# Optimization experiments

Measured on AMD Instinct MI355X. Metric: run time of the kernel, lower is better.

## Reference

```python
import jax, jax.numpy as jnp
import numpy as np

Q = 8192      # num query tokens
S = 32768     # num support points
E = 131072    # num edges (query<-support neighbor pairs)
D = 256       # token_dim
H = 8         # num_heads
HD = D // H   # head_dim = 32
GEO = 128     # geo mlp_hidden = geo_dim
FFN = 2 * D   # ffn hidden
STAT_IN = 12  # 4 stats * 3 coords
EPS_LN = 1e-5


def gelu(x):
    return jax.nn.gelu(x, approximate=False)  # torch nn.GELU default (erf)


def layernorm(x, g, b):
    m = jnp.mean(x, axis=-1, keepdims=True)
    v = jnp.mean((x - m) ** 2, axis=-1, keepdims=True)
    return (x - m) * jax.lax.rsqrt(v + EPS_LN) * g + b


def setup_inputs() -> dict:
    key = jax.random.key(0)
    ks = jax.random.split(key, 16)
    w = lambda k, shp: jax.random.normal(k, shp, jnp.float32) * 0.02
    return {
        "query_tokens": jax.random.normal(ks[0], (Q, D), jnp.float32),
        "query_pos": jax.random.normal(ks[1], (Q, 3), jnp.float32),
        "support_feats": jax.random.normal(ks[2], (S, D), jnp.float32),
        "support_pos": jax.random.normal(ks[3], (S, 3), jnp.float32),
        "Wq": w(ks[4], (D, D)), "Wk": w(ks[5], (D, D)), "Wv": w(ks[6], (D, D)),
        "Wg": w(ks[7], (GEO, D)),
        "Wo": w(ks[8], (D, D)), "bo": jnp.zeros((D,), jnp.float32),
        "log_tau": jnp.array(0.0, jnp.float32),
        "ln1_g": jnp.ones((D,), jnp.float32), "ln1_b": jnp.zeros((D,), jnp.float32),
        "ln2_g": jnp.ones((D,), jnp.float32), "ln2_b": jnp.zeros((D,), jnp.float32),
        "Wf1": w(ks[9], (D, FFN)), "bf1": jnp.zeros((FFN,), jnp.float32),
        "Wf2": w(ks[10], (FFN, D)), "bf2": jnp.zeros((D,), jnp.float32),
        "Gw1": w(ks[11], (STAT_IN, GEO)), "Gb1": jnp.zeros((GEO,), jnp.float32),
        "Gw2": w(ks[12], (GEO, GEO)), "Gb2": jnp.zeros((GEO,), jnp.float32),
        "q_idx": jnp.sort(jax.random.randint(ks[13], (E,), 0, Q)),
        "s_idx": jax.random.randint(ks[14], (E,), 0, S),
        "num_queries": Q,
    }


def geo_stats(rel, q_idx, num_q):
    # rel: [E,3] relative positions; segmented mean/std/min/max -> [num_q, 12]
    ones = jnp.ones((rel.shape[0], 1), rel.dtype)
    cnt = jnp.maximum(jax.ops.segment_sum(ones, q_idx, num_q), 1.0)  # [Q,1]
    mean = jax.ops.segment_sum(rel, q_idx, num_q) / cnt
    var = jax.ops.segment_sum((rel - mean[q_idx]) ** 2, q_idx, num_q) / cnt
    std = jnp.sqrt(var)
    # torch inits min/max with +/-inf then clamps to [-100,100]; jax segment
    # min/max init with dtype extremes -> same result after clip
    mn = jnp.clip(jax.ops.segment_min(rel, q_idx, num_q), -100.0, 100.0)
    mx = jnp.clip(jax.ops.segment_max(rel, q_idx, num_q), -100.0, 100.0)
    return jnp.concatenate([mean, std, mn, mx], axis=-1)


def reference(query_tokens, query_pos, support_feats, support_pos,
              Wq, Wk, Wv, Wg, Wo, bo, log_tau,
              ln1_g, ln1_b, ln2_g, ln2_b,
              Wf1, bf1, Wf2, bf2, Gw1, Gb1, Gw2, Gb2,
              q_idx, s_idx, num_queries):
    num_q = num_queries
    # ---- statistical geo embedding ----
    rel = support_pos[s_idx] - query_pos[q_idx]                 # [E,3]
    raw = geo_stats(rel, q_idx, num_q)                          # [Q,12]
    geo = gelu(gelu(raw @ Gw1 + Gb1) @ Gw2 + Gb2)               # [Q,GEO]

    # ---- AGNO cross attention (pre-norm) ----
    qt = layernorm(query_tokens, ln1_g, ln1_b)
    Qf = qt @ Wq                                                # [Q,D]
    Kf = support_feats @ Wk                                     # [S,D]
    Vf = support_feats @ Wv                                     # [S,D]
    Gf = geo @ Wg                                               # [Q,D]
    qh = Qf[q_idx].reshape(E, H, HD)
    kh = Kf[s_idx].reshape(E, H, HD)
    vh = Vf[s_idx].reshape(E, H, HD)
    gh = Gf[q_idx].reshape(E, H, HD)
    tau = jnp.exp(log_tau)
    scores = jnp.sum(qh * kh, axis=-1) / (jnp.sqrt(jnp.float32(HD)) * tau)  # [E,H]
    # torch scores_max starts at 0 -> max(0, segment max)
    smax = jnp.maximum(jax.ops.segment_max(scores, q_idx, num_q), 0.0)
    ex = jnp.exp(scores - smax[q_idx])
    ssum = jax.ops.segment_sum(ex, q_idx, num_q)
    alpha = ex / jnp.maximum(ssum[q_idx], 1e-8)                 # [E,H]
    weighted = alpha[..., None] * (vh + gh)                     # [E,H,HD]
    out = jax.ops.segment_sum(weighted, q_idx, num_q)           # [Q,H,HD]
    attn = out.reshape(num_q, D) @ Wo + bo

    # ---- residual + FFN ----
    x = query_tokens + attn
    x = x + gelu(layernorm(x, ln2_g, ln2_b) @ Wf1 + bf1) @ Wf2 + bf2
    return x
```

## Files before the change

### kernel.cpp

```cpp
#include <hip/hip_runtime.h>
#include <math.h>

#define QN 8192
#define SN 32768
#define EN 131072
#define DN 256
#define HN 8
#define HDN 32
#define GEON 128
#define FFNN 512

typedef __attribute__((ext_vector_type(8))) short bf16x8;
typedef __attribute__((ext_vector_type(8))) unsigned short u16x8;
typedef __attribute__((ext_vector_type(4))) float f32x4;

__device__ __forceinline__ unsigned short f2b(float f) {
  union { float f; unsigned u; } v; v.f = f;
  unsigned u = v.u;
  u += 0x7fffu + ((u >> 16) & 1u);
  return (unsigned short)(u >> 16);
}
__device__ __forceinline__ float b2f(unsigned short h) {
  union { unsigned u; float f; } v; v.u = ((unsigned)h) << 16; return v.f;
}
__device__ __forceinline__ float gelu_f(float x) {
  return 0.5f * x * (1.0f + erff(x * 0.70710678118654752440f));
}

template <int KT>
__device__ __forceinline__ u16x8* lds_gk(unsigned short* base, int row, int col) {
  int g = (col >> 3) ^ (row & 7);
  return reinterpret_cast<u16x8*>(base + row * KT + g * 8);
}
__device__ __forceinline__ unsigned short* lds_gs128(unsigned short* base, int row, int col) {
  int g = (col >> 3) ^ (row & 7);
  return base + row * 128 + g * 8 + (col & 7);
}

__global__ __launch_bounds__(256) void fused_prep(
    const float* Wq, const float* Wk, const float* Wv, const float* Wg,
    const float* Wo, const float* Wf1, const float* Wf2,
    unsigned short* WqT, unsigned short* WkvT, unsigned short* WgT,
    unsigned short* WoT, unsigned short* Wf1T, unsigned short* Wf2T,
    const int* q_idx, int* offs,
    const float* x_ln, const float* lng, const float* lnb, unsigned short* ln_out) {
  __shared__ float ts[64][65];
  int b = blockIdx.x;
  int t = threadIdx.x;
  if (b < 136) {
    const float* src; unsigned short* dst; int K, N, tile;
    if (b < 16)       { src = Wq;  dst = WqT;          K = 256; N = 256; tile = b; }
    else if (b < 32)  { src = Wk;  dst = WkvT;         K = 256; N = 256; tile = b - 16; }
    else if (b < 48)  { src = Wv;  dst = WkvT + 65536; K = 256; N = 256; tile = b - 32; }
    else if (b < 56)  { src = Wg;  dst = WgT;          K = 128; N = 256; tile = b - 48; }
    else if (b < 72)  { src = Wo;  dst = WoT;          K = 256; N = 256; tile = b - 56; }
    else if (b < 104) { src = Wf1; dst = Wf1T;         K = 256; N = 512; tile = b - 72; }
    else              { src = Wf2; dst = Wf2T;         K = 512; N = 256; tile = b - 104; }
    int ktiles = K >> 6;
    int k0 = (tile % ktiles) * 64, n0 = (tile / ktiles) * 64;
    int c4 = (t & 15) * 4;
    int r = t >> 4;
#pragma unroll
    for (int p = 0; p < 4; ++p) {
      int row = p * 16 + r;
      float4 v = *(const float4*)(src + (size_t)(k0 + row) * N + n0 + c4);
      ts[row][c4 + 0] = v.x; ts[row][c4 + 1] = v.y;
      ts[row][c4 + 2] = v.z; ts[row][c4 + 3] = v.w;
    }
    __syncthreads();
#pragma unroll
    for (int p = 0; p < 4; ++p) {
      int n = p * 16 + r;
      ushort4 o;
      o.x = f2b(ts[c4 + 0][n]); o.y = f2b(ts[c4 + 1][n]);
      o.z = f2b(ts[c4 + 2][n]); o.w = f2b(ts[c4 + 3][n]);
      *(ushort4*)(dst + (size_t)(n0 + n) * K + k0 + c4) = o;
    }
  } else if (b < 169) {
    int i = (b - 136) * 256 + t;
    if (i > QN) return;
    int lo = 0, hi = EN;
    while (lo < hi) {
      int mid = (lo + hi) >> 1;
      if (q_idx[mid] < i) lo = mid + 1; else hi = mid;
    }
    offs[i] = lo;
  } else {
    int row = (b - 169) * 4 + (t >> 6);
    int lane = t & 63;
    const float* xr = x_ln + (size_t)row * DN;
    float4 v = *(const float4*)(xr + lane * 4);
    float s = v.x + v.y + v.z + v.w;
    float ss = v.x * v.x + v.y * v.y + v.z * v.z + v.w * v.w;
#pragma unroll
    for (int msk = 1; msk <= 32; msk <<= 1) {
      s += __shfl_xor(s, msk);
      ss += __shfl_xor(ss, msk);
    }
    float mean = s * (1.f / 256.f);
    float var = ss * (1.f / 256.f) - mean * mean;
    float rs = 1.0f / sqrtf(var + 1e-5f);
    float4 gg = *(const float4*)(lng + lane * 4);
    float4 bb = *(const float4*)(lnb + lane * 4);
    unsigned short* o = ln_out + (size_t)row * DN + lane * 4;
    o[0] = f2b((v.x - mean) * rs * gg.x + bb.x);
    o[1] = f2b((v.y - mean) * rs * gg.y + bb.y);
    o[2] = f2b((v.z - mean) * rs * gg.z + bb.z);
    o[3] = f2b((v.w - mean) * rs * gg.w + bb.w);
  }
}

__global__ __launch_bounds__(256) void ln_kernel(
    const float* x, const float* g, const float* b, unsigned short* out) {
  int row = blockIdx.x * 4 + (threadIdx.x >> 6);
  int lane = threadIdx.x & 63;
  const float* xr = x + (size_t)row * DN;
  float4 v = *(const float4*)(xr + lane * 4);
  float s = v.x + v.y + v.z + v.w;
  float ss = v.x * v.x + v.y * v.y + v.z * v.z + v.w * v.w;
#pragma unroll
  for (int msk = 1; msk <= 32; msk <<= 1) {
    s += __shfl_xor(s, msk);
    ss += __shfl_xor(ss, msk);
  }
  float mean = s * (1.f / 256.f);
  float var = ss * (1.f / 256.f) - mean * mean;
  float rs = 1.0f / sqrtf(var + 1e-5f);
  float4 gg = *(const float4*)(g + lane * 4);
  float4 bb = *(const float4*)(b + lane * 4);
  unsigned short* o = out + (size_t)row * DN + lane * 4;
  o[0] = f2b((v.x - mean) * rs * gg.x + bb.x);
  o[1] = f2b((v.y - mean) * rs * gg.y + bb.y);
  o[2] = f2b((v.z - mean) * rs * gg.z + bb.z);
  o[3] = f2b((v.w - mean) * rs * gg.w + bb.w);
}


__device__ __forceinline__ void kv_body(
    char* smem, const float* A, const unsigned short* BT, unsigned short* KVb,
    int bm, int t) {
  unsigned short* As = (unsigned short*)smem;
  unsigned short* Bs = (unsigned short*)(smem + 32768);
  int w = t >> 6, lane = t & 63;
  int quad = lane >> 4, l16 = lane & 15;
  int wr = w >> 1, wc = w & 1;
  {
    int prow = t >> 6;
    int c4 = (t & 63) * 4;
#pragma unroll
    for (int p = 0; p < 16; ++p) {
      int lr = p * 4 + prow;
      float4 f = *(const float4*)(A + (size_t)(bm + lr) * 256 + c4);
      ushort4 u;
      u.x = f2b(f.x); u.y = f2b(f.y); u.z = f2b(f.z); u.w = f2b(f.w);
      int g = (c4 >> 3) ^ (lr & 7);
      *(ushort4*)(As + lr * 256 + g * 8 + (c4 & 7)) = u;
    }
  }
  int brow = t >> 3, bsub = t & 7;
  u16x8 pre[4];
  {
    const unsigned short* Bg = BT + (size_t)brow * 256 + bsub * 32;
#pragma unroll
    for (int i = 0; i < 4; ++i) pre[i] = *reinterpret_cast<const u16x8*>(Bg + i * 8);
  }
  for (int ct = 0; ct < 16; ++ct) {
#pragma unroll
    for (int i = 0; i < 4; ++i)
      *lds_gk<256>(Bs, brow, bsub * 32 + i * 8) = pre[i];
    __syncthreads();
    if (ct < 15) {
      const unsigned short* Bg = BT + (size_t)((ct + 1) * 32 + brow) * 256 + bsub * 32;
#pragma unroll
      for (int i = 0; i < 4; ++i) pre[i] = *reinterpret_cast<const u16x8*>(Bg + i * 8);
    }
    f32x4 acc[2];
    acc[0] = (f32x4){0.f, 0.f, 0.f, 0.f};
    acc[1] = (f32x4){0.f, 0.f, 0.f, 0.f};
#pragma unroll
    for (int k = 0; k < 8; ++k) {
      bf16x8 a0 = *reinterpret_cast<bf16x8*>(lds_gk<256>(As, wr * 32 + l16, k * 32 + quad * 8));
      bf16x8 a1 = *reinterpret_cast<bf16x8*>(lds_gk<256>(As, wr * 32 + 16 + l16, k * 32 + quad * 8));
      bf16x8 b0 = *reinterpret_cast<bf16x8*>(lds_gk<256>(Bs, wc * 16 + l16, k * 32 + quad * 8));
      acc[0] = __builtin_amdgcn_mfma_f32_16x16x32_bf16(a0, b0, acc[0], 0, 0, 0);
      acc[1] = __builtin_amdgcn_mfma_f32_16x16x32_bf16(a1, b0, acc[1], 0, 0, 0);
    }
#pragma unroll
    for (int i = 0; i < 2; ++i)
#pragma unroll
      for (int r = 0; r < 4; ++r) {
        int rw = bm + wr * 32 + i * 16 + quad * 4 + r;
        int col = ct * 32 + wc * 16 + l16;
        KVb[(size_t)rw * 512 + col] = f2b(acc[i][r]);
      }
    __syncthreads();
  }
}

template <bool A_FP32, bool HAS_BIAS, bool DO_GELU, bool HAS_RESID, bool STORE_F32>
__device__ __forceinline__ void gemm64_body(
    char* smem, const void* Ap, const unsigned short* BT, int N, int K,
    const float* bias, const float* resid, float* outF, unsigned short* outB,
    int bm, int bn, int t) {
  unsigned short (*As)[40] = (unsigned short(*)[40])smem;
  unsigned short (*Bs)[40] = (unsigned short(*)[40])(smem + 5120);
  int w = t >> 6, lane = t & 63;
  int wr = w >> 1, wc = w & 1;
  int quad = lane >> 4, l16 = lane & 15;
  int row = t >> 2, chunk = t & 3;

  const float* AgF = (const float*)Ap + (size_t)(bm + row) * K + chunk * 8;
  const unsigned short* AgB = (const unsigned short*)Ap + (size_t)(bm + row) * K + chunk * 8;
  const unsigned short* Bg = BT + (size_t)(bn + row) * K + chunk * 8;

  float4 pf0, pf1;
  u16x8 pa, pb;
  if (A_FP32) { pf0 = *(const float4*)AgF; pf1 = *(const float4*)(AgF + 4); }
  else        { pa = *(const u16x8*)AgB; }
  pb = *(const u16x8*)Bg;

  f32x4 acc[2][2];
#pragma unroll
  for (int i = 0; i < 2; ++i)
#pragma unroll
    for (int j = 0; j < 2; ++j) acc[i][j] = (f32x4){0.f, 0.f, 0.f, 0.f};

  for (int k0 = 0; k0 < K; k0 += 32) {
    u16x8 ua;
    if (A_FP32) {
      ua[0] = f2b(pf0.x); ua[1] = f2b(pf0.y); ua[2] = f2b(pf0.z); ua[3] = f2b(pf0.w);
      ua[4] = f2b(pf1.x); ua[5] = f2b(pf1.y); ua[6] = f2b(pf1.z); ua[7] = f2b(pf1.w);
    } else {
      ua = pa;
    }
    *reinterpret_cast<u16x8*>(&As[row][chunk * 8]) = ua;
    *reinterpret_cast<u16x8*>(&Bs[row][chunk * 8]) = pb;
    __syncthreads();
    if (k0 + 32 < K) {
      if (A_FP32) { pf0 = *(const float4*)(AgF + k0 + 32); pf1 = *(const float4*)(AgF + k0 + 36); }
      else        { pa = *(const u16x8*)(AgB + k0 + 32); }
      pb = *(const u16x8*)(Bg + k0 + 32);
    }
    bf16x8 a0 = *reinterpret_cast<const bf16x8*>(&As[wr * 32 + l16][quad * 8]);
    bf16x8 a1 = *reinterpret_cast<const bf16x8*>(&As[wr * 32 + 16 + l16][quad * 8]);
    bf16x8 b0 = *reinterpret_cast<const bf16x8*>(&Bs[wc * 32 + l16][quad * 8]);
    bf16x8 b1 = *reinterpret_cast<const bf16x8*>(&Bs[wc * 32 + 16 + l16][quad * 8]);
    acc[0][0] = __builtin_amdgcn_mfma_f32_16x16x32_bf16(a0, b0, acc[0][0], 0, 0, 0);
    acc[0][1] = __builtin_amdgcn_mfma_f32_16x16x32_bf16(a0, b1, acc[0][1], 0, 0, 0);
    acc[1][0] = __builtin_amdgcn_mfma_f32_16x16x32_bf16(a1, b0, acc[1][0], 0, 0, 0);
    acc[1][1] = __builtin_amdgcn_mfma_f32_16x16x32_bf16(a1, b1, acc[1][1], 0, 0, 0);
    __syncthreads();
  }

#pragma unroll
  for (int i = 0; i < 2; ++i)
#pragma unroll
    for (int j = 0; j < 2; ++j) {
      int col = bn + wc * 32 + j * 16 + l16;
      float bv = HAS_BIAS ? bias[col] : 0.f;
#pragma unroll
      for (int r = 0; r < 4; ++r) {
        int rw = bm + wr * 32 + i * 16 + quad * 4 + r;
        float v = acc[i][j][r] + bv;
        if (DO_GELU) v = gelu_f(v);
        if (HAS_RESID) v += resid[(size_t)rw * N + col];
        if (STORE_F32) outF[(size_t)rw * N + col] = v;
        else outB[(size_t)rw * N + col] = f2b(v);
      }
    }
}

__device__ __forceinline__ void geo_body(
    char* smem, const float* qpos, const float* spos, const int* offs,
    const int* s_idx, const float* Gw1, const float* Gb1,
    const float* Gw2, const float* Gb2, const unsigned short* WgT,
    unsigned short* Gf_b, int qb, int t) {
  float (*rs)[12] = (float(*)[12])smem;
  unsigned short* geoL = (unsigned short*)(smem + 3072);
  float (*h1)[128] = (float(*)[128])(smem + 19456);
  unsigned short* Bs = (unsigned short*)(smem + 19456);

  {
    int q = qb + (t >> 2);
    int sub = t & 3;
    int e0 = offs[q], e1 = offs[q + 1];
    float qx = qpos[q * 3 + 0], qy = qpos[q * 3 + 1], qz = qpos[q * 3 + 2];
    float cnt = 0.f, sx = 0.f, sy = 0.f, sz = 0.f, sxx = 0.f, syy = 0.f, szz = 0.f;
    float mnx = 1e30f, mny = 1e30f, mnz = 1e30f, mxx = -1e30f, mxy = -1e30f, mxz = -1e30f;
    for (int e = e0 + sub; e < e1; e += 4) {
      int s = s_idx[e];
      float rx = spos[s * 3 + 0] - qx;
      float ry = spos[s * 3 + 1] - qy;
      float rz = spos[s * 3 + 2] - qz;
      cnt += 1.f;
      sx += rx; sy += ry; sz += rz;
      sxx += rx * rx; syy += ry * ry; szz += rz * rz;
      mnx = fminf(mnx, rx); mny = fminf(mny, ry); mnz = fminf(mnz, rz);
      mxx = fmaxf(mxx, rx); mxy = fmaxf(mxy, ry); mxz = fmaxf(mxz, rz);
    }
#pragma unroll
    for (int msk = 1; msk <= 2; msk <<= 1) {
      cnt += __shfl_xor(cnt, msk);
      sx += __shfl_xor(sx, msk); sy += __shfl_xor(sy, msk); sz += __shfl_xor(sz, msk);
      sxx += __shfl_xor(sxx, msk); syy += __shfl_xor(syy, msk); szz += __shfl_xor(szz, msk);
      mnx = fminf(mnx, __shfl_xor(mnx, msk));
      mny = fminf(mny, __shfl_xor(mny, msk));
      mnz = fminf(mnz, __shfl_xor(mnz, msk));
      mxx = fmaxf(mxx, __shfl_xor(mxx, msk));
      mxy = fmaxf(mxy, __shfl_xor(mxy, msk));
      mxz = fmaxf(mxz, __shfl_xor(mxz, msk));
    }
    if (sub == 0) {
      int qq = t >> 2;
      float c = fmaxf(cnt, 1.f);
      float mx_ = sx / c, my_ = sy / c, mz_ = sz / c;
      float vx = fmaxf(sxx / c - mx_ * mx_, 0.f);
      float vy = fmaxf(syy / c - my_ * my_, 0.f);
      float vz = fmaxf(szz / c - mz_ * mz_, 0.f);
      rs[qq][0] = mx_; rs[qq][1] = my_; rs[qq][2] = mz_;
      rs[qq][3] = sqrtf(vx); rs[qq][4] = sqrtf(vy); rs[qq][5] = sqrtf(vz);
      rs[qq][6] = fminf(fmaxf(mnx, -100.f), 100.f);
      rs[qq][7] = fminf(fmaxf(mny, -100.f), 100.f);
      rs[qq][8] = fminf(fmaxf(mnz, -100.f), 100.f);
      rs[qq][9] = fminf(fmaxf(mxx, -100.f), 100.f);
      rs[qq][10] = fminf(fmaxf(mxy, -100.f), 100.f);
      rs[qq][11] = fminf(fmaxf(mxz, -100.f), 100.f);
    }
  }
  __syncthreads();

  {
    int j = t & 127;
    int grp = t >> 7;
    int qbase = grp * 32;
    float acc[32];
    float b1 = Gb1[j];
#pragma unroll
    for (int qq = 0; qq < 32; ++qq) acc[qq] = b1;
    for (int i = 0; i < 12; ++i) {
      float wv = Gw1[i * GEON + j];
#pragma unroll
      for (int qq = 0; qq < 32; ++qq) acc[qq] += rs[qbase + qq][i] * wv;
    }
#pragma unroll
    for (int qq = 0; qq < 32; ++qq) h1[qbase + qq][j] = gelu_f(acc[qq]);
    __syncthreads();
    float b2 = Gb2[j];
    float acc2[32];
#pragma unroll
    for (int qq = 0; qq < 32; ++qq) acc2[qq] = b2;
    for (int k = 0; k < 128; ++k) {
      float wv = Gw2[k * GEON + j];
#pragma unroll
      for (int qq = 0; qq < 32; ++qq) acc2[qq] += h1[qbase + qq][k] * wv;
    }
#pragma unroll
    for (int qq = 0; qq < 32; ++qq)
      *lds_gs128(geoL, qbase + qq, j) = f2b(gelu_f(acc2[qq]));
  }
  __syncthreads();

  {
    int w = t >> 6, lane = t & 63;
    int wr = w >> 1, wc = w & 1;
    int quad = lane >> 4, l16 = lane & 15;
    int row = t >> 2, sub = t & 3;
    for (int ct = 0; ct < 4; ++ct) {
      int bn = ct * 64;
      {
        const unsigned short* Bg = WgT + (size_t)(bn + row) * 128 + sub * 32;
#pragma unroll
        for (int i = 0; i < 4; ++i)
          *lds_gk<128>(Bs, row, sub * 32 + i * 8) = *reinterpret_cast<const u16x8*>(Bg + i * 8);
      }
      __syncthreads();
      f32x4 acc[2][2];
#pragma unroll
      for (int i = 0; i < 2; ++i)
#pragma unroll
        for (int j = 0; j < 2; ++j) acc[i][j] = (f32x4){0.f, 0.f, 0.f, 0.f};
#pragma unroll
      for (int k = 0; k < 4; ++k) {
        bf16x8 a0 = *reinterpret_cast<bf16x8*>(lds_gk<128>(geoL, wr * 32 + l16, k * 32 + quad * 8));
        bf16x8 a1 = *reinterpret_cast<bf16x8*>(lds_gk<128>(geoL, wr * 32 + 16 + l16, k * 32 + quad * 8));
        bf16x8 b0 = *reinterpret_cast<bf16x8*>(lds_gk<128>(Bs, wc * 32 + l16, k * 32 + quad * 8));
        bf16x8 b1 = *reinterpret_cast<bf16x8*>(lds_gk<128>(Bs, wc * 32 + 16 + l16, k * 32 + quad * 8));
        acc[0][0] = __builtin_amdgcn_mfma_f32_16x16x32_bf16(a0, b0, acc[0][0], 0, 0, 0);
        acc[0][1] = __builtin_amdgcn_mfma_f32_16x16x32_bf16(a0, b1, acc[0][1], 0, 0, 0);
        acc[1][0] = __builtin_amdgcn_mfma_f32_16x16x32_bf16(a1, b0, acc[1][0], 0, 0, 0);
        acc[1][1] = __builtin_amdgcn_mfma_f32_16x16x32_bf16(a1, b1, acc[1][1], 0, 0, 0);
      }
#pragma unroll
      for (int i = 0; i < 2; ++i)
#pragma unroll
        for (int j = 0; j < 2; ++j) {
          int col = bn + wc * 32 + j * 16 + l16;
#pragma unroll
          for (int r = 0; r < 4; ++r) {
            int rw = qb + wr * 32 + i * 16 + quad * 4 + r;
            Gf_b[(size_t)rw * 256 + col] = f2b(acc[i][j][r]);
          }
        }
      __syncthreads();
    }
  }
}

__global__ __launch_bounds__(256) void fused_stage2(
    const float* qpos, const float* spos, const int* offs, const int* s_idx,
    const float* Gw1, const float* Gb1, const float* Gw2, const float* Gb2,
    const unsigned short* WgT, unsigned short* Gf_b,
    const float* support_feats, const unsigned short* WkvT, unsigned short* KVb,
    const unsigned short* qt_b, const unsigned short* WqT, unsigned short* Qb) {
  __shared__ __align__(16) char smem[52224];
  int b = blockIdx.x;
  int t = threadIdx.x;
  if (b < 128) {
    geo_body(smem, qpos, spos, offs, s_idx, Gw1, Gb1, Gw2, Gb2, WgT, Gf_b, b * 64, t);
  } else if (b < 640) {
    kv_body(smem, support_feats, WkvT, KVb, (b - 128) * 64, t);
  } else {
    int bb = b - 640;
    int bm = (bb & 127) * 64, bn = (bb >> 7) * 64;
    gemm64_body<false, false, false, false, false>(
        smem, qt_b, WqT, DN, 256, nullptr, nullptr, nullptr, Qb, bm, bn, t);
  }
}

template <bool A_FP32, bool HAS_BIAS, bool DO_GELU, bool HAS_RESID, bool STORE_F32>
__global__ __launch_bounds__(256) void gemm64(
    const void* Ap, const unsigned short* BT, int N, int K,
    const float* bias, const float* resid, float* outF, unsigned short* outB) {
  __shared__ __align__(16) char smem[10240];
  gemm64_body<A_FP32, HAS_BIAS, DO_GELU, HAS_RESID, STORE_F32>(
      smem, Ap, BT, N, K, bias, resid, outF, outB,
      blockIdx.x * 64, blockIdx.y * 64, threadIdx.x);
}

__global__ __launch_bounds__(256) void attn_edge_kernel(
    const unsigned short* Qb, const unsigned short* Gfb, const unsigned short* KVb,
    const int* s_idx, const int* offs, const float* log_tau, unsigned short* attn_b) {
  int q = blockIdx.x * 4 + (threadIdx.x >> 6);
  int lane = threadIdx.x & 63;
  int slot = lane >> 4;
  int sl = lane & 15;
  int d0 = sl * 16;
  int e0 = offs[q], e1 = offs[q + 1];
  float invs = expf(-log_tau[0]) * 0.17677669529663687f;
  u16x8 qu0 = *(const u16x8*)(Qb + (size_t)q * DN + d0);
  u16x8 qu1 = *(const u16x8*)(Qb + (size_t)q * DN + d0 + 8);
  u16x8 gu0 = *(const u16x8*)(Gfb + (size_t)q * DN + d0);
  u16x8 gu1 = *(const u16x8*)(Gfb + (size_t)q * DN + d0 + 8);
  float qf[16], gf[16];
#pragma unroll
  for (int j = 0; j < 8; ++j) {
    qf[j] = b2f(qu0[j]) * invs; qf[j + 8] = b2f(qu1[j]) * invs;
    gf[j] = b2f(gu0[j]);        gf[j + 8] = b2f(gu1[j]);
  }
  const float NEG = -1e30f;
  float m = -INFINITY, l = 0.f;
  float a[16];
#pragma unroll
  for (int j = 0; j < 16; ++j) a[j] = 0.f;
  for (int e = e0; e < e1; e += 4) {
    int ee = e + slot;
    bool valid = ee < e1;
    int s = s_idx[valid ? ee : (e1 - 1)];
    const unsigned short* kr = KVb + (size_t)s * 512 + d0;
    u16x8 ku0 = *(const u16x8*)kr;
    u16x8 ku1 = *(const u16x8*)(kr + 8);
    u16x8 vu0 = *(const u16x8*)(kr + 256);
    u16x8 vu1 = *(const u16x8*)(kr + 264);
    float p = 0.f;
#pragma unroll
    for (int j = 0; j < 8; ++j) {
      p += qf[j] * b2f(ku0[j]);
      p += qf[j + 8] * b2f(ku1[j]);
    }
    p += __shfl_xor(p, 1);
    if (!valid) p = -INFINITY;
    float mnew = fmaxf(m, p);
    float sc = (m > NEG) ? __expf(m - mnew) : 0.f;
    float we = valid ? __expf(p - mnew) : 0.f;
    l = l * sc + we;
#pragma unroll
    for (int j = 0; j < 8; ++j) {
      a[j] = a[j] * sc + we * b2f(vu0[j]);
      a[j + 8] = a[j + 8] * sc + we * b2f(vu1[j]);
    }
    m = mnew;
  }
#pragma unroll
  for (int msk = 16; msk <= 32; msk <<= 1) {
    float om = __shfl_xor(m, msk);
    float ol = __shfl_xor(l, msk);
    float M2 = fmaxf(m, om);
    float ws = (m > NEG) ? __expf(m - M2) : 0.f;
    float wo = (om > NEG) ? __expf(om - M2) : 0.f;
    l = l * ws + ol * wo;
#pragma unroll
    for (int j = 0; j < 16; ++j) {
      float oa = __shfl_xor(a[j], msk);
      a[j] = a[j] * ws + oa * wo;
    }
    m = M2;
  }
  float M = fmaxf(m, 0.f);
  float em = (m > NEG) ? __expf(m - M) : 0.f;
  float denom = fmaxf(l * em, 1e-8f);
  float f = em / denom;
  float sa = l * f;
  if (slot == 0) {
    u16x8 o0, o1;
#pragma unroll
    for (int j = 0; j < 8; ++j) {
      o0[j] = f2b(a[j] * f + gf[j] * sa);
      o1[j] = f2b(a[j + 8] * f + gf[j + 8] * sa);
    }
    *(u16x8*)(attn_b + (size_t)q * DN + d0) = o0;
    *(u16x8*)(attn_b + (size_t)q * DN + d0 + 8) = o1;
  }
}

extern "C" void kernel_launch(void* const* d_in, const int* in_sizes, int n_in,
                              void* d_out, int out_size, void* d_ws, size_t ws_size,
                              hipStream_t stream) {
  const float* query_tokens  = (const float*)d_in[0];
  const float* query_pos     = (const float*)d_in[1];
  const float* support_feats = (const float*)d_in[2];
  const float* support_pos   = (const float*)d_in[3];
  const float* Wq  = (const float*)d_in[4];
  const float* Wk  = (const float*)d_in[5];
  const float* Wv  = (const float*)d_in[6];
  const float* Wg  = (const float*)d_in[7];
  const float* Wo  = (const float*)d_in[8];
  const float* bo  = (const float*)d_in[9];
  const float* log_tau = (const float*)d_in[10];
  const float* ln1_g = (const float*)d_in[11];
  const float* ln1_b = (const float*)d_in[12];
  const float* ln2_g = (const float*)d_in[13];
  const float* ln2_b = (const float*)d_in[14];
  const float* Wf1 = (const float*)d_in[15];
  const float* bf1 = (const float*)d_in[16];
  const float* Wf2 = (const float*)d_in[17];
  const float* bf2 = (const float*)d_in[18];
  const float* Gw1 = (const float*)d_in[19];
  const float* Gb1 = (const float*)d_in[20];
  const float* Gw2 = (const float*)d_in[21];
  const float* Gb2 = (const float*)d_in[22];
  const int* q_idx = (const int*)d_in[23];
  const int* s_idx = (const int*)d_in[24];
  float* out = (float*)d_out;

  char* ws = (char*)d_ws;
  size_t off = 0;
  auto alloc = [&](size_t bytes) -> void* {
    void* p = ws + off;
    off = (off + bytes + 255) & ~(size_t)255;
    return p;
  };
  unsigned short* WqT  = (unsigned short*)alloc(65536 * 2);
  unsigned short* WkvT = (unsigned short*)alloc(131072 * 2);
  unsigned short* WgT  = (unsigned short*)alloc(32768 * 2);
  unsigned short* WoT  = (unsigned short*)alloc(65536 * 2);
  unsigned short* Wf1T = (unsigned short*)alloc(131072 * 2);
  unsigned short* Wf2T = (unsigned short*)alloc(131072 * 2);
  int* offs            = (int*)alloc((QN + 1) * 4);
  unsigned short* qt_b  = (unsigned short*)alloc((size_t)QN * DN * 2);
  unsigned short* Qb    = (unsigned short*)alloc((size_t)QN * DN * 2);
  unsigned short* Gf_b  = (unsigned short*)alloc((size_t)QN * DN * 2);
  unsigned short* KVb   = (unsigned short*)alloc((size_t)SN * 512 * 2);
  unsigned short* attn_b = (unsigned short*)alloc((size_t)QN * DN * 2);
  float* x1             = (float*)alloc((size_t)QN * DN * 4);
  unsigned short* z_b   = (unsigned short*)alloc((size_t)QN * DN * 2);
  unsigned short* h_b   = (unsigned short*)alloc((size_t)QN * FFNN * 2);

  fused_prep<<<2217, 256, 0, stream>>>(Wq, Wk, Wv, Wg, Wo, Wf1, Wf2,
                                       WqT, WkvT, WgT, WoT, Wf1T, Wf2T,
                                       q_idx, offs,
                                       query_tokens, ln1_g, ln1_b, qt_b);
  fused_stage2<<<1152, 256, 0, stream>>>(query_pos, support_pos, offs, s_idx,
                                         Gw1, Gb1, Gw2, Gb2, WgT, Gf_b,
                                         support_feats, WkvT, KVb,
                                         qt_b, WqT, Qb);
  attn_edge_kernel<<<QN / 4, 256, 0, stream>>>(Qb, Gf_b, KVb, s_idx, offs, log_tau, attn_b);
  gemm64<false, true, false, true, true><<<dim3(QN / 64, DN / 64), 256, 0, stream>>>(
      attn_b, WoT, DN, 256, bo, query_tokens, x1, nullptr);
  ln_kernel<<<QN / 4, 256, 0, stream>>>(x1, ln2_g, ln2_b, z_b);
  gemm64<false, true, true, false, false><<<dim3(QN / 64, FFNN / 64), 256, 0, stream>>>(
      z_b, Wf1T, FFNN, 256, bf1, nullptr, nullptr, h_b);
  gemm64<false, true, false, true, true><<<dim3(QN / 64, DN / 64), 256, 0, stream>>>(
      h_b, Wf2T, DN, 512, bf2, x1, out, nullptr);

  (void)in_sizes; (void)n_in; (void)out_size; (void)ws_size;
}
```

Baseline: 240.9 us.

## Fuse FFN GEMMs into one kernel and prefetch KV rows in attention loop

The two FFN GEMMs are replaced by one kernel. Each block computes a 16-row slice of the GELU hidden activations into LDS and immediately multiplies it by Wf2, adding bias and residual, so the bf16 hidden tensor never goes to global memory. Separately, the per-query attention edge loop now software-pipelines the gather: it loads the next iteration's K/V rows and the s_idx value after that before computing the current one, to hide gather latency. The fused FFN reads weight B fragments straight from global/L2 without LDS staging and runs small 16-row tiles, which raises weight traffic per block. The prefetch adds register pressure.

```diff
diff --git a/kernel.cpp b/kernel.cpp
--- a/kernel.cpp
+++ b/kernel.cpp
@@ -35,6 +35,10 @@
 __device__ __forceinline__ unsigned short* lds_gs128(unsigned short* base, int row, int col) {
   int g = (col >> 3) ^ (row & 7);
   return base + row * 128 + g * 8 + (col & 7);
+}
+__device__ __forceinline__ unsigned short* lds_gs512(unsigned short* base, int row, int col) {
+  int g = (col >> 3) ^ (row & 7);
+  return base + row * 512 + g * 8 + (col & 7);
 }
 
 __global__ __launch_bounds__(256) void fused_prep(
@@ -437,6 +441,79 @@
       blockIdx.x * 64, blockIdx.y * 64, threadIdx.x);
 }
 
+__global__ __launch_bounds__(256) void ffn_kernel(
+    const unsigned short* z_b, const unsigned short* Wf1T, const float* bf1,
+    const unsigned short* Wf2T, const float* bf2, const float* x1, float* out) {
+  __shared__ __align__(16) char smem[8192 + 16384];
+  unsigned short* Zs = (unsigned short*)smem;
+  unsigned short* Hs = (unsigned short*)(smem + 8192);
+  int t = threadIdx.x;
+  int bm = blockIdx.x * 16;
+  int w = t >> 6, lane = t & 63;
+  int quad = lane >> 4, l16 = lane & 15;
+  {
+    int row = t >> 4, sub = t & 15;
+    const unsigned short* Zg = z_b + (size_t)(bm + row) * 256 + sub * 16;
+    *lds_gk<256>(Zs, row, sub * 16) = *(const u16x8*)Zg;
+    *lds_gk<256>(Zs, row, sub * 16 + 8) = *(const u16x8*)(Zg + 8);
+  }
+  __syncthreads();
+#pragma unroll
+  for (int tile = 0; tile < 2; ++tile) {
+    int cb = w * 128 + tile * 64;
+    f32x4 acc[4];
+#pragma unroll
+    for (int j = 0; j < 4; ++j) acc[j] = (f32x4){0.f, 0.f, 0.f, 0.f};
+#pragma unroll
+    for (int k = 0; k < 8; ++k) {
+      bf16x8 a = *reinterpret_cast<bf16x8*>(lds_gk<256>(Zs, l16, k * 32 + quad * 8));
+#pragma unroll
+      for (int j = 0; j < 4; ++j) {
+        bf16x8 b = *reinterpret_cast<const bf16x8*>(
+            Wf1T + (size_t)(cb + j * 16 + l16) * 256 + k * 32 + quad * 8);
+        acc[j] = __builtin_amdgcn_mfma_f32_16x16x32_bf16(a, b, acc[j], 0, 0, 0);
+      }
+    }
+#pragma unroll
+    for (int j = 0; j < 4; ++j) {
+      int col = cb + j * 16 + l16;
+      float bv = bf1[col];
+#pragma unroll
+      for (int r = 0; r < 4; ++r) {
+        int row = quad * 4 + r;
+        *lds_gs512(Hs, row, col) = f2b(gelu_f(acc[j][r] + bv));
+      }
+    }
+  }
+  __syncthreads();
+  {
+    int cb = w * 64;
+    f32x4 acc[4];
+#pragma unroll
+    for (int j = 0; j < 4; ++j) acc[j] = (f32x4){0.f, 0.f, 0.f, 0.f};
+#pragma unroll
+    for (int k = 0; k < 16; ++k) {
+      bf16x8 a = *reinterpret_cast<bf16x8*>(lds_gk<512>(Hs, l16, k * 32 + quad * 8));
+#pragma unroll
+      for (int j = 0; j < 4; ++j) {
+        bf16x8 b = *reinterpret_cast<const bf16x8*>(
+            Wf2T + (size_t)(cb + j * 16 + l16) * 512 + k * 32 + quad * 8);
+        acc[j] = __builtin_amdgcn_mfma_f32_16x16x32_bf16(a, b, acc[j], 0, 0, 0);
+      }
+    }
+#pragma unroll
+    for (int j = 0; j < 4; ++j) {
+      int col = cb + j * 16 + l16;
+      float bv = bf2[col];
+#pragma unroll
+      for (int r = 0; r < 4; ++r) {
+        int rw = bm + quad * 4 + r;
+        out[(size_t)rw * 256 + col] = acc[j][r] + bv + x1[(size_t)rw * 256 + col];
+      }
+    }
+  }
+}
+
 __global__ __launch_bounds__(256) void attn_edge_kernel(
     const unsigned short* Qb, const unsigned short* Gfb, const unsigned short* KVb,
     const int* s_idx, const int* offs, const float* log_tau, unsigned short* attn_b) {
@@ -462,20 +539,32 @@
   float a[16];
 #pragma unroll
   for (int j = 0; j < 16; ++j) a[j] = 0.f;
+
+  int sNxt = 0;
+  u16x8 cku0, cku1, cvu0, cvu1;
+  if (e0 < e1) {
+    int i0 = e0 + slot; if (i0 > e1 - 1) i0 = e1 - 1;
+    int sCur = s_idx[i0];
+    if (e0 + 4 < e1) { int i1 = e0 + 4 + slot; if (i1 > e1 - 1) i1 = e1 - 1; sNxt = s_idx[i1]; }
+    const unsigned short* kr = KVb + (size_t)sCur * 512 + d0;
+    cku0 = *(const u16x8*)kr;        cku1 = *(const u16x8*)(kr + 8);
+    cvu0 = *(const u16x8*)(kr + 256); cvu1 = *(const u16x8*)(kr + 264);
+  }
   for (int e = e0; e < e1; e += 4) {
-    int ee = e + slot;
-    bool valid = ee < e1;
-    int s = s_idx[valid ? ee : (e1 - 1)];
-    const unsigned short* kr = KVb + (size_t)s * 512 + d0;
-    u16x8 ku0 = *(const u16x8*)kr;
-    u16x8 ku1 = *(const u16x8*)(kr + 8);
-    u16x8 vu0 = *(const u16x8*)(kr + 256);
-    u16x8 vu1 = *(const u16x8*)(kr + 264);
+    bool hasNext = (e + 4 < e1);
+    u16x8 nku0, nku1, nvu0, nvu1;
+    if (hasNext) {
+      const unsigned short* krn = KVb + (size_t)sNxt * 512 + d0;
+      nku0 = *(const u16x8*)krn;        nku1 = *(const u16x8*)(krn + 8);
+      nvu0 = *(const u16x8*)(krn + 256); nvu1 = *(const u16x8*)(krn + 264);
+      if (e + 8 < e1) { int i2 = e + 8 + slot; if (i2 > e1 - 1) i2 = e1 - 1; sNxt = s_idx[i2]; }
+    }
+    bool valid = (e + slot) < e1;
     float p = 0.f;
 #pragma unroll
     for (int j = 0; j < 8; ++j) {
-      p += qf[j] * b2f(ku0[j]);
-      p += qf[j + 8] * b2f(ku1[j]);
+      p += qf[j] * b2f(cku0[j]);
+      p += qf[j + 8] * b2f(cku1[j]);
     }
     p += __shfl_xor(p, 1);
     if (!valid) p = -INFINITY;
@@ -485,10 +574,11 @@
     l = l * sc + we;
 #pragma unroll
     for (int j = 0; j < 8; ++j) {
-      a[j] = a[j] * sc + we * b2f(vu0[j]);
-      a[j + 8] = a[j + 8] * sc + we * b2f(vu1[j]);
+      a[j] = a[j] * sc + we * b2f(cvu0[j]);
+      a[j + 8] = a[j + 8] * sc + we * b2f(cvu1[j]);
     }
     m = mnew;
+    if (hasNext) { cku0 = nku0; cku1 = nku1; cvu0 = nvu0; cvu1 = nvu1; }
   }
 #pragma unroll
   for (int msk = 16; msk <= 32; msk <<= 1) {
@@ -573,7 +663,6 @@
   unsigned short* attn_b = (unsigned short*)alloc((size_t)QN * DN * 2);
   float* x1             = (float*)alloc((size_t)QN * DN * 4);
   unsigned short* z_b   = (unsigned short*)alloc((size_t)QN * DN * 2);
-  unsigned short* h_b   = (unsigned short*)alloc((size_t)QN * FFNN * 2);
 
   fused_prep<<<2217, 256, 0, stream>>>(Wq, Wk, Wv, Wg, Wo, Wf1, Wf2,
                                        WqT, WkvT, WgT, WoT, Wf1T, Wf2T,
@@ -587,10 +676,7 @@
   gemm64<false, true, false, true, true><<<dim3(QN / 64, DN / 64), 256, 0, stream>>>(
       attn_b, WoT, DN, 256, bo, query_tokens, x1, nullptr);
   ln_kernel<<<QN / 4, 256, 0, stream>>>(x1, ln2_g, ln2_b, z_b);
-  gemm64<false, true, true, false, false><<<dim3(QN / 64, FFNN / 64), 256, 0, stream>>>(
-      z_b, Wf1T, FFNN, 256, bf1, nullptr, nullptr, h_b);
-  gemm64<false, true, false, true, true><<<dim3(QN / 64, DN / 64), 256, 0, stream>>>(
-      h_b, Wf2T, DN, 512, bf2, x1, out, nullptr);
+  ffn_kernel<<<QN / 16, 256, 0, stream>>>(z_b, Wf1T, bf1, Wf2T, bf2, x1, out);
 
   (void)in_sizes; (void)n_in; (void)out_size; (void)ws_size;
 }
```

Result: slower. 258.7 us (+7.4%).
